# Kernel tuning notes

Hardware: AMD Instinct MI355X
Metric: run time of the kernel (lower is better)

## Reference

```python
import jax, jax.numpy as jnp
import numpy as np

N_EXP, N_EMBD = 8, 1024
D_FF = 4 * N_EMBD
TOK = 2048  # tokens per expert


def setup_inputs() -> dict:
    key = jax.random.key(0)
    k_x, k_fc, k_pr, k_fb, k_pb = jax.random.split(key, 5)
    scale = 0.02
    return {
        "x": jax.random.normal(k_x, (N_EXP, TOK, N_EMBD), dtype=jnp.float32),
        "c_fc": jax.random.normal(k_fc, (N_EXP, N_EMBD, D_FF), dtype=jnp.float32) * scale,
        "c_proj": jax.random.normal(k_pr, (N_EXP, D_FF, N_EMBD), dtype=jnp.float32) * scale,
        "fc_bias": jax.random.normal(k_fb, (N_EXP, 1, D_FF), dtype=jnp.float32) * scale,
        "proj_bias": jax.random.normal(k_pb, (N_EXP, 1, N_EMBD), dtype=jnp.float32) * scale,
    }


def reference(x, c_fc, c_proj, fc_bias, proj_bias):
    # grouped GEMM over experts: [e, t, d] @ [e, d, f] -> [e, t, f]
    h = jnp.einsum('etd,edf->etf', x, c_fc) + fc_bias
    h = jax.nn.gelu(h, approximate=False)  # torch nn.GELU default is exact erf
    out = jnp.einsum('etf,efd->etd', h, c_proj) + proj_bias
    # dropout p=0.0 (eval): identity
    return out
```

## Files before the change

### kernel.cpp

```cpp
#include <hip/hip_runtime.h>
#include <cmath>

typedef __bf16 bf16;
typedef __bf16 bf16x8 __attribute__((ext_vector_type(8)));
typedef float floatx4 __attribute__((ext_vector_type(4)));

#define E_ 8
#define M_ 2048
#define D_ 1024
#define F_ 4096

#define PUNROLL _Pragma("unroll")

__device__ __forceinline__ void async16(const void* g, void* l) {
    __builtin_amdgcn_global_load_lds((const __attribute__((address_space(1))) unsigned int*)g,
                                     (__attribute__((address_space(3))) unsigned int*)l, 16, 0, 0);
}

__device__ __forceinline__ float gelu_fast(float u) {
    float s = u * (-1.5957691216f - 0.0713548162726f * u * u);
    return u * __builtin_amdgcn_rcpf(1.0f + __expf(s));
}

__device__ __forceinline__ void tconv_body(const float* __restrict__ in, bf16* __restrict__ out,
                                           int R, int C, int bx, int by, int bz,
                                           float (*t)[65]) {
    size_t eoff = (size_t)bz * R * C;
    in += eoff;
    out += eoff;
    const int c0 = bx * 64, r0 = by * 64;
    const int tid = threadIdx.x;
    const int f4c = tid & 15;
    const int rsub = tid >> 4;
    PUNROLL
    for (int p = 0; p < 4; ++p) {
        int row = rsub + p * 16;
        float4 v = *(const float4*)&in[(size_t)(r0 + row) * C + c0 + f4c * 4];
        t[row][f4c * 4 + 0] = v.x;
        t[row][f4c * 4 + 1] = v.y;
        t[row][f4c * 4 + 2] = v.z;
        t[row][f4c * 4 + 3] = v.w;
    }
    __syncthreads();
    const int rr = (tid & 7) * 8;
    const int cbase = tid >> 3;
    PUNROLL
    for (int p = 0; p < 2; ++p) {
        int c = cbase + p * 32;
        bf16x8 o = {(bf16)t[rr + 0][c], (bf16)t[rr + 1][c], (bf16)t[rr + 2][c],
                    (bf16)t[rr + 3][c], (bf16)t[rr + 4][c], (bf16)t[rr + 5][c],
                    (bf16)t[rr + 6][c], (bf16)t[rr + 7][c]};
        *(bf16x8*)&out[(size_t)(c0 + c) * R + r0 + rr] = o;
    }
}

__global__ __launch_bounds__(256) void prep_kernel(const float4* __restrict__ x,
                                                   bf16x8* __restrict__ xb,
                                                   const float* __restrict__ c_fc,
                                                   bf16* __restrict__ w1T) {
    __shared__ float t[64][65];
    const int b = blockIdx.x;
    if (b < 2048) {
        const int n8 = E_ * M_ * D_ / 8;
        int i = b * 256 + threadIdx.x;
        for (; i < n8; i += 2048 * 256) {
            float4 a = x[2 * i], c = x[2 * i + 1];
            bf16x8 r = {(bf16)a.x, (bf16)a.y, (bf16)a.z, (bf16)a.w,
                        (bf16)c.x, (bf16)c.y, (bf16)c.z, (bf16)c.w};
            xb[i] = r;
        }
    } else {
        const int idx = b - 2048;
        tconv_body(c_fc, w1T, D_, F_, idx & 63, (idx >> 6) & 15, idx >> 10, t);
    }
}

__global__ __launch_bounds__(256) void tconv2_kernel(const float* __restrict__ in,
                                                     bf16* __restrict__ out) {
    __shared__ float t[64][65];
    const int idx = blockIdx.x;
    tconv_body(in, out, F_, D_, idx & 15, (idx >> 4) & 63, idx >> 10, t);
}

template <bool GELU>
__global__ __launch_bounds__(512, 2) void gemm256(const bf16* __restrict__ A,
                                                  const bf16* __restrict__ Bt,
                                                  const float* __restrict__ bias,
                                                  void* __restrict__ Out,
                                                  int M, int N, int K) {
    extern __shared__ __align__(16) char sm[];
    const int nt = K >> 6;
    const int NTm = M >> 8;
    const int NTn = N >> 8;
    const int nwg = gridDim.x;
    const int bid = blockIdx.x;
    const int swz = (bid & 7) * (nwg >> 3) + (bid >> 3);
    const int tm = swz % NTm;
    const int tn = (swz / NTm) % NTn;
    const int e = swz / (NTm * NTn);
    A += (size_t)e * M * K;
    Bt += (size_t)e * N * K;
    bias += (size_t)e * N;
    const int row0 = tm << 8;
    const int col0 = tn << 8;

    const int tid = threadIdx.x;
    const int l = tid & 63;
    const int w = tid >> 6;
    const int wm = w >> 2;
    const int wn = w & 3;

    const size_t Kb = (size_t)K * 2;
    const size_t half128 = 128 * Kb;
    const size_t j64 = 64 * Kb;
    const int srow = (w << 3) + (l >> 3);
    const int kb = ((l & 7) ^ ((l >> 3) & 7)) << 4;
    const char* aSrc = (const char*)A + (size_t)(row0 + srow) * Kb + kb;
    const char* bSrc = (const char*)Bt + (size_t)(col0 + srow) * Kb + kb;
    const int ldsW = w << 10;

    auto stage = [&](int hb, const char* src, int ko) {
        async16(src + ko, sm + hb + ldsW);
        async16(src + j64 + ko, sm + hb + 8192 + ldsW);
    };

    const int kpat0 = (((l >> 4) << 4)) ^ ((l & 7) << 4);
    const int kpat1 = (64 + ((l >> 4) << 4)) ^ ((l & 7) << 4);
    const int aRowOff = (((wm << 6) + (l & 15)) << 7);
    const int bRowOff = (((wn << 5) + (l & 15)) << 7);

    bf16x8 aa[4][2];
    bf16x8 bb0[2][2], bb1[2][2];
    floatx4 acc00[4][2] = {}, acc01[4][2] = {}, acc10[4][2] = {}, acc11[4][2] = {};

#define READ_A(QM)                                                                          \
    PUNROLL                                                                                 \
    for (int mi = 0; mi < 4; ++mi) {                                                        \
        aa[mi][0] = *(const bf16x8*)(sm + p + (QM)*16384 + aRowOff + mi * 2048 + kpat0);    \
        aa[mi][1] = *(const bf16x8*)(sm + p + (QM)*16384 + aRowOff + mi * 2048 + kpat1);    \
    }
#define READ_B(BB, QN)                                                                      \
    PUNROLL                                                                                 \
    for (int ni = 0; ni < 2; ++ni) {                                                        \
        BB[ni][0] = *(const bf16x8*)(sm + p + 32768 + (QN)*16384 + bRowOff + ni * 2048 + kpat0); \
        BB[ni][1] = *(const bf16x8*)(sm + p + 32768 + (QN)*16384 + bRowOff + ni * 2048 + kpat1); \
    }
#define MQ(ACC, BB)                                                                         \
    PUNROLL                                                                                 \
    for (int mi = 0; mi < 4; ++mi) PUNROLL for (int ni = 0; ni < 2; ++ni) {                 \
        ACC[mi][ni] = __builtin_amdgcn_mfma_f32_16x16x32_bf16(aa[mi][0], BB[ni][0], ACC[mi][ni], 0, 0, 0); \
        ACC[mi][ni] = __builtin_amdgcn_mfma_f32_16x16x32_bf16(aa[mi][1], BB[ni][1], ACC[mi][ni], 0, 0, 0); \
    }

    stage(0, aSrc, 0);
    stage(32768, bSrc, 0);
    stage(49152, bSrc + half128, 0);
    stage(16384, aSrc + half128, 0);
    stage(65536 + 0, aSrc, 128);
    stage(65536 + 32768, bSrc, 128);
    stage(65536 + 49152, bSrc + half128, 128);
    asm volatile("s_waitcnt vmcnt(6)" ::: "memory");
    __builtin_amdgcn_s_barrier();

    for (int t = 0; t < nt; ++t) {
        const int p = (t & 1) << 16;
        const int pn = p ^ 65536;
        const int ko1 = (t + 1) << 7;
        const int ko2 = (t + 2) << 7;
        READ_A(0)
        READ_B(bb0, 0)
        if (t + 1 < nt) stage(pn + 16384, aSrc + half128, ko1);
        __builtin_amdgcn_s_barrier();
        __builtin_amdgcn_s_setprio(1);
        MQ(acc00, bb0)
        __builtin_amdgcn_s_setprio(0);
        __builtin_amdgcn_s_barrier();
        READ_B(bb1, 1)
        if (t + 2 < nt) stage(p + 0, aSrc, ko2);
        __builtin_amdgcn_s_barrier();
        __builtin_amdgcn_s_setprio(1);
        MQ(acc01, bb1)
        __builtin_amdgcn_s_setprio(0);
        __builtin_amdgcn_s_barrier();
        READ_A(1)
        if (t + 2 < nt) stage(p + 32768, bSrc, ko2);
        __builtin_amdgcn_s_barrier();
        __builtin_amdgcn_s_setprio(1);
        MQ(acc11, bb1)
        __builtin_amdgcn_s_setprio(0);
        __builtin_amdgcn_s_barrier();
        if (t + 2 < nt) {
            stage(p + 49152, bSrc + half128, ko2);
            asm volatile("s_waitcnt vmcnt(6)" ::: "memory");
        } else if (t + 1 < nt) {
            asm volatile("s_waitcnt vmcnt(0)" ::: "memory");
        }
        __builtin_amdgcn_s_barrier();
        __builtin_amdgcn_s_setprio(1);
        MQ(acc10, bb0)
        __builtin_amdgcn_s_setprio(0);
        __builtin_amdgcn_s_barrier();
    }

    const size_t outBase = (size_t)e * M * N;
#define EPI(ACC, QM, QN)                                                                    \
    PUNROLL                                                                                 \
    for (int ni = 0; ni < 2; ++ni) {                                                        \
        const int col = col0 + (QN)*128 + (wn << 5) + ni * 16 + (l & 15);                   \
        const float bv = bias[col];                                                         \
        PUNROLL                                                                             \
        for (int mi = 0; mi < 4; ++mi) {                                                    \
            const int row = row0 + (QM)*128 + (wm << 6) + mi * 16 + ((l >> 4) << 2);        \
            PUNROLL                                                                         \
            for (int r = 0; r < 4; ++r) {                                                   \
                float v = ACC[mi][ni][r] + bv;                                              \
                if (GELU)                                                                   \
                    ((bf16*)Out)[outBase + (size_t)(row + r) * N + col] = (bf16)gelu_fast(v); \
                else                                                                        \
                    ((float*)Out)[outBase + (size_t)(row + r) * N + col] = v;               \
            }                                                                               \
        }                                                                                   \
    }
    EPI(acc00, 0, 0)
    EPI(acc01, 0, 1)
    EPI(acc11, 1, 1)
    EPI(acc10, 1, 0)
#undef READ_A
#undef READ_B
#undef MQ
#undef EPI
}

extern "C" void kernel_launch(void* const* d_in, const int* in_sizes, int n_in,
                              void* d_out, int out_size, void* d_ws, size_t ws_size,
                              hipStream_t stream) {
    const float* x = (const float*)d_in[0];
    const float* c_fc = (const float*)d_in[1];
    const float* c_proj = (const float*)d_in[2];
    const float* fc_bias = (const float*)d_in[3];
    const float* proj_bias = (const float*)d_in[4];
    float* out = (float*)d_out;

    bf16* xb = (bf16*)d_ws;
    bf16* wT = xb + (size_t)E_ * M_ * D_;
    bf16* h = wT + (size_t)E_ * D_ * F_;
    size_t need = ((size_t)E_ * M_ * D_ + (size_t)E_ * D_ * F_ + (size_t)E_ * M_ * F_) * 2;
    if (ws_size < need) return;

    static bool attrDone = false;
    if (!attrDone) {
        (void)hipFuncSetAttribute((const void*)&gemm256<true>,
                                  hipFuncAttributeMaxDynamicSharedMemorySize, 131072);
        (void)hipFuncSetAttribute((const void*)&gemm256<false>,
                                  hipFuncAttributeMaxDynamicSharedMemorySize, 131072);
        attrDone = true;
    }

    prep_kernel<<<10240, 256, 0, stream>>>((const float4*)x, (bf16x8*)xb, c_fc, wT);
    gemm256<true><<<1024, 512, 131072, stream>>>(xb, wT, fc_bias, h, M_, F_, D_);
    tconv2_kernel<<<8192, 256, 0, stream>>>(c_proj, wT);
    gemm256<false><<<256, 512, 131072, stream>>>(h, wT, proj_bias, out, M_, D_, F_);
}
```

Before: 613.3 us.

## Make GEMM persistent over tiles with overlapped next-tile prologue; fuse weight prep

The first GEMM now launches 256 workgroups that each loop over 4 output tiles. Each workgroup issues the async LDS prologue loads for its next tile before running the epilogue of the current one, so global loads overlap the output stores. When the workspace is large enough, both weight transposes and the x conversion are fused into one prep launch, which removes a kernel launch and the serialization between the GEMMs. The costs are tile-ordering and cache-locality changes from the new swizzle, plus extra workspace for a second transposed weight buffer.

```diff
diff --git a/kernel.cpp b/kernel.cpp
--- a/kernel.cpp
+++ b/kernel.cpp
@@ -54,6 +54,37 @@
     }
 }
 
+__device__ __forceinline__ void xconv_body(const float4* __restrict__ x, bf16x8* __restrict__ xb,
+                                           int b, int nblk) {
+    const int n8 = E_ * M_ * D_ / 8;
+    int i = b * 256 + threadIdx.x;
+    for (; i < n8; i += nblk * 256) {
+        float4 a = x[2 * i], c = x[2 * i + 1];
+        bf16x8 r = {(bf16)a.x, (bf16)a.y, (bf16)a.z, (bf16)a.w,
+                    (bf16)c.x, (bf16)c.y, (bf16)c.z, (bf16)c.w};
+        xb[i] = r;
+    }
+}
+
+__global__ __launch_bounds__(256) void prep_all(const float4* __restrict__ x,
+                                                bf16x8* __restrict__ xb,
+                                                const float* __restrict__ c_fc,
+                                                bf16* __restrict__ w1T,
+                                                const float* __restrict__ c_proj,
+                                                bf16* __restrict__ w2T) {
+    __shared__ float t[64][65];
+    const int b = blockIdx.x;
+    if (b < 2048) {
+        xconv_body(x, xb, b, 2048);
+    } else if (b < 10240) {
+        const int idx = b - 2048;
+        tconv_body(c_fc, w1T, D_, F_, idx & 63, (idx >> 6) & 15, idx >> 10, t);
+    } else {
+        const int idx = b - 10240;
+        tconv_body(c_proj, w2T, F_, D_, idx & 15, (idx >> 4) & 63, idx >> 10, t);
+    }
+}
+
 __global__ __launch_bounds__(256) void prep_kernel(const float4* __restrict__ x,
                                                    bf16x8* __restrict__ xb,
                                                    const float* __restrict__ c_fc,
@@ -61,14 +92,7 @@
     __shared__ float t[64][65];
     const int b = blockIdx.x;
     if (b < 2048) {
-        const int n8 = E_ * M_ * D_ / 8;
-        int i = b * 256 + threadIdx.x;
-        for (; i < n8; i += 2048 * 256) {
-            float4 a = x[2 * i], c = x[2 * i + 1];
-            bf16x8 r = {(bf16)a.x, (bf16)a.y, (bf16)a.z, (bf16)a.w,
-                        (bf16)c.x, (bf16)c.y, (bf16)c.z, (bf16)c.w};
-            xb[i] = r;
-        }
+        xconv_body(x, xb, b, 2048);
     } else {
         const int idx = b - 2048;
         tconv_body(c_fc, w1T, D_, F_, idx & 63, (idx >> 6) & 15, idx >> 10, t);
@@ -83,11 +107,11 @@
 }
 
 template <bool GELU>
-__global__ __launch_bounds__(512, 2) void gemm256(const bf16* __restrict__ A,
-                                                  const bf16* __restrict__ Bt,
-                                                  const float* __restrict__ bias,
+__global__ __launch_bounds__(512, 2) void gemm256(const bf16* __restrict__ A0,
+                                                  const bf16* __restrict__ Bt0,
+                                                  const float* __restrict__ bias0,
                                                   void* __restrict__ Out,
-                                                  int M, int N, int K) {
+                                                  int M, int N, int K, int tpb) {
     extern __shared__ __align__(16) char sm[];
     const int nt = K >> 6;
     const int NTm = M >> 8;
@@ -95,14 +119,6 @@
     const int nwg = gridDim.x;
     const int bid = blockIdx.x;
     const int swz = (bid & 7) * (nwg >> 3) + (bid >> 3);
-    const int tm = swz % NTm;
-    const int tn = (swz / NTm) % NTn;
-    const int e = swz / (NTm * NTn);
-    A += (size_t)e * M * K;
-    Bt += (size_t)e * N * K;
-    bias += (size_t)e * N;
-    const int row0 = tm << 8;
-    const int col0 = tn << 8;
 
     const int tid = threadIdx.x;
     const int l = tid & 63;
@@ -115,23 +131,42 @@
     const size_t j64 = 64 * Kb;
     const int srow = (w << 3) + (l >> 3);
     const int kb = ((l & 7) ^ ((l >> 3) & 7)) << 4;
-    const char* aSrc = (const char*)A + (size_t)(row0 + srow) * Kb + kb;
-    const char* bSrc = (const char*)Bt + (size_t)(col0 + srow) * Kb + kb;
     const int ldsW = w << 10;
 
     auto stage = [&](int hb, const char* src, int ko) {
         async16(src + ko, sm + hb + ldsW);
         async16(src + j64 + ko, sm + hb + 8192 + ldsW);
     };
+    auto prologue = [&](const char* aS, const char* bS) {
+        stage(0, aS, 0);
+        stage(32768, bS, 0);
+        stage(49152, bS + half128, 0);
+        stage(16384, aS + half128, 0);
+        stage(65536 + 0, aS, 128);
+        stage(65536 + 32768, bS, 128);
+        stage(65536 + 49152, bS + half128, 128);
+    };
 
     const int kpat0 = (((l >> 4) << 4)) ^ ((l & 7) << 4);
     const int kpat1 = (64 + ((l >> 4) << 4)) ^ ((l & 7) << 4);
     const int aRowOff = (((wm << 6) + (l & 15)) << 7);
     const int bRowOff = (((wn << 5) + (l & 15)) << 7);
 
-    bf16x8 aa[4][2];
-    bf16x8 bb0[2][2], bb1[2][2];
-    floatx4 acc00[4][2] = {}, acc01[4][2] = {}, acc10[4][2] = {}, acc11[4][2] = {};
+    int tile = swz * tpb;
+    int tm = tile % NTm, rem = tile / NTm;
+    int tn = rem % NTn, e = rem / NTn;
+    int row0 = tm << 8, col0 = tn << 8;
+    const char* aS = (const char*)A0 + ((size_t)e * M + row0 + srow) * Kb + kb;
+    const char* bS = (const char*)Bt0 + ((size_t)e * N + col0 + srow) * Kb + kb;
+    prologue(aS, bS);
+
+    for (int j = 0; j < tpb; ++j) {
+        asm volatile("s_waitcnt vmcnt(6)" ::: "memory");
+        __builtin_amdgcn_s_barrier();
+
+        bf16x8 aa[4][2];
+        bf16x8 bb0[2][2], bb1[2][2];
+        floatx4 acc00[4][2] = {}, acc01[4][2] = {}, acc10[4][2] = {}, acc11[4][2] = {};
 
 #define READ_A(QM)                                                                          \
     PUNROLL                                                                                 \
@@ -152,83 +187,86 @@
         ACC[mi][ni] = __builtin_amdgcn_mfma_f32_16x16x32_bf16(aa[mi][1], BB[ni][1], ACC[mi][ni], 0, 0, 0); \
     }
 
-    stage(0, aSrc, 0);
-    stage(32768, bSrc, 0);
-    stage(49152, bSrc + half128, 0);
-    stage(16384, aSrc + half128, 0);
-    stage(65536 + 0, aSrc, 128);
-    stage(65536 + 32768, bSrc, 128);
-    stage(65536 + 49152, bSrc + half128, 128);
-    asm volatile("s_waitcnt vmcnt(6)" ::: "memory");
-    __builtin_amdgcn_s_barrier();
-
-    for (int t = 0; t < nt; ++t) {
-        const int p = (t & 1) << 16;
-        const int pn = p ^ 65536;
-        const int ko1 = (t + 1) << 7;
-        const int ko2 = (t + 2) << 7;
-        READ_A(0)
-        READ_B(bb0, 0)
-        if (t + 1 < nt) stage(pn + 16384, aSrc + half128, ko1);
-        __builtin_amdgcn_s_barrier();
-        __builtin_amdgcn_s_setprio(1);
-        MQ(acc00, bb0)
-        __builtin_amdgcn_s_setprio(0);
-        __builtin_amdgcn_s_barrier();
-        READ_B(bb1, 1)
-        if (t + 2 < nt) stage(p + 0, aSrc, ko2);
-        __builtin_amdgcn_s_barrier();
-        __builtin_amdgcn_s_setprio(1);
-        MQ(acc01, bb1)
-        __builtin_amdgcn_s_setprio(0);
-        __builtin_amdgcn_s_barrier();
-        READ_A(1)
-        if (t + 2 < nt) stage(p + 32768, bSrc, ko2);
-        __builtin_amdgcn_s_barrier();
-        __builtin_amdgcn_s_setprio(1);
-        MQ(acc11, bb1)
-        __builtin_amdgcn_s_setprio(0);
-        __builtin_amdgcn_s_barrier();
-        if (t + 2 < nt) {
-            stage(p + 49152, bSrc + half128, ko2);
-            asm volatile("s_waitcnt vmcnt(6)" ::: "memory");
-        } else if (t + 1 < nt) {
-            asm volatile("s_waitcnt vmcnt(0)" ::: "memory");
+        for (int t = 0; t < nt; ++t) {
+            const int p = (t & 1) << 16;
+            const int pn = p ^ 65536;
+            const int ko1 = (t + 1) << 7;
+            const int ko2 = (t + 2) << 7;
+            READ_A(0)
+            READ_B(bb0, 0)
+            if (t + 1 < nt) stage(pn + 16384, aS + half128, ko1);
+            __builtin_amdgcn_s_barrier();
+            __builtin_amdgcn_s_setprio(1);
+            MQ(acc00, bb0)
+            __builtin_amdgcn_s_setprio(0);
+            __builtin_amdgcn_s_barrier();
+            READ_B(bb1, 1)
+            if (t + 2 < nt) stage(p + 0, aS, ko2);
+            __builtin_amdgcn_s_barrier();
+            __builtin_amdgcn_s_setprio(1);
+            MQ(acc01, bb1)
+            __builtin_amdgcn_s_setprio(0);
+            __builtin_amdgcn_s_barrier();
+            READ_A(1)
+            if (t + 2 < nt) stage(p + 32768, bS, ko2);
+            __builtin_amdgcn_s_barrier();
+            __builtin_amdgcn_s_setprio(1);
+            MQ(acc11, bb1)
+            __builtin_amdgcn_s_setprio(0);
+            __builtin_amdgcn_s_barrier();
+            if (t + 2 < nt) {
+                stage(p + 49152, bS + half128, ko2);
+                asm volatile("s_waitcnt vmcnt(6)" ::: "memory");
+            } else if (t + 1 < nt) {
+                asm volatile("s_waitcnt vmcnt(0)" ::: "memory");
+            }
+            __builtin_amdgcn_s_barrier();
+            __builtin_amdgcn_s_setprio(1);
+            MQ(acc10, bb0)
+            __builtin_amdgcn_s_setprio(0);
+            __builtin_amdgcn_s_barrier();
         }
-        __builtin_amdgcn_s_barrier();
-        __builtin_amdgcn_s_setprio(1);
-        MQ(acc10, bb0)
-        __builtin_amdgcn_s_setprio(0);
-        __builtin_amdgcn_s_barrier();
-    }
-
-    const size_t outBase = (size_t)e * M * N;
+
+        const int erow0 = row0, ecol0 = col0;
+        const float* ebias = bias0 + (size_t)e * N;
+        const size_t eout = (size_t)e * M * N;
+        if (j + 1 < tpb) {
+            tile = swz * tpb + j + 1;
+            tm = tile % NTm; rem = tile / NTm;
+            tn = rem % NTn; e = rem / NTn;
+            row0 = tm << 8; col0 = tn << 8;
+            aS = (const char*)A0 + ((size_t)e * M + row0 + srow) * Kb + kb;
+            bS = (const char*)Bt0 + ((size_t)e * N + col0 + srow) * Kb + kb;
+            prologue(aS, bS);
+        }
+
 #define EPI(ACC, QM, QN)                                                                    \
     PUNROLL                                                                                 \
     for (int ni = 0; ni < 2; ++ni) {                                                        \
-        const int col = col0 + (QN)*128 + (wn << 5) + ni * 16 + (l & 15);                   \
-        const float bv = bias[col];                                                         \
+        const int col = ecol0 + (QN)*128 + (wn << 5) + ni * 16 + (l & 15);                  \
+        const float bv = ebias[col];                                                        \
         PUNROLL                                                                             \
         for (int mi = 0; mi < 4; ++mi) {                                                    \
-            const int row = row0 + (QM)*128 + (wm << 6) + mi * 16 + ((l >> 4) << 2);        \
+            const int row = erow0 + (QM)*128 + (wm << 6) + mi * 16 + ((l >> 4) << 2);       \
             PUNROLL                                                                         \
             for (int r = 0; r < 4; ++r) {                                                   \
                 float v = ACC[mi][ni][r] + bv;                                              \
                 if (GELU)                                                                   \
-                    ((bf16*)Out)[outBase + (size_t)(row + r) * N + col] = (bf16)gelu_fast(v); \
+                    ((bf16*)Out)[eout + (size_t)(row + r) * N + col] = (bf16)gelu_fast(v);  \
                 else                                                                        \
-                    ((float*)Out)[outBase + (size_t)(row + r) * N + col] = v;               \
+                    ((float*)Out)[eout + (size_t)(row + r) * N + col] = v;                  \
             }                                                                               \
         }                                                                                   \
     }
-    EPI(acc00, 0, 0)
-    EPI(acc01, 0, 1)
-    EPI(acc11, 1, 1)
-    EPI(acc10, 1, 0)
+        EPI(acc00, 0, 0)
+        EPI(acc01, 0, 1)
+        EPI(acc11, 1, 1)
+        EPI(acc10, 1, 0)
 #undef READ_A
 #undef READ_B
 #undef MQ
 #undef EPI
+    }
 }
 
 extern "C" void kernel_launch(void* const* d_in, const int* in_sizes, int n_in,
@@ -241,11 +279,12 @@
     const float* proj_bias = (const float*)d_in[4];
     float* out = (float*)d_out;
 
-    bf16* xb = (bf16*)d_ws;
-    bf16* wT = xb + (size_t)E_ * M_ * D_;
-    bf16* h = wT + (size_t)E_ * D_ * F_;
-    size_t need = ((size_t)E_ * M_ * D_ + (size_t)E_ * D_ * F_ + (size_t)E_ * M_ * F_) * 2;
-    if (ws_size < need) return;
+    const size_t EMD = (size_t)E_ * M_ * D_;
+    const size_t EDF = (size_t)E_ * D_ * F_;
+    const size_t EMF = (size_t)E_ * M_ * F_;
+    const size_t need1 = (EMD + EDF + EMF) * 2;
+    const size_t need2 = (EMD + 2 * EDF + EMF) * 2;
+    if (ws_size < need1) return;
 
     static bool attrDone = false;
     if (!attrDone) {
@@ -256,8 +295,21 @@
         attrDone = true;
     }
 
-    prep_kernel<<<10240, 256, 0, stream>>>((const float4*)x, (bf16x8*)xb, c_fc, wT);
-    gemm256<true><<<1024, 512, 131072, stream>>>(xb, wT, fc_bias, h, M_, F_, D_);
-    tconv2_kernel<<<8192, 256, 0, stream>>>(c_proj, wT);
-    gemm256<false><<<256, 512, 131072, stream>>>(h, wT, proj_bias, out, M_, D_, F_);
-}
+    bf16* xb = (bf16*)d_ws;
+    bf16* w1T = xb + EMD;
+
+    if (ws_size >= need2) {
+        bf16* w2T = w1T + EDF;
+        bf16* h = w2T + EDF;
+        prep_all<<<18432, 256, 0, stream>>>((const float4*)x, (bf16x8*)xb, c_fc, w1T,
+                                            c_proj, w2T);
+        gemm256<true><<<256, 512, 131072, stream>>>(xb, w1T, fc_bias, h, M_, F_, D_, 4);
+        gemm256<false><<<256, 512, 131072, stream>>>(h, w2T, proj_bias, out, M_, D_, F_, 1);
+    } else {
+        bf16* h = w1T + EDF;
+        prep_kernel<<<10240, 256, 0, stream>>>((const float4*)x, (bf16x8*)xb, c_fc, w1T);
+        gemm256<true><<<256, 512, 131072, stream>>>(xb, w1T, fc_bias, h, M_, F_, D_, 4);
+        tconv2_kernel<<<8192, 256, 0, stream>>>(c_proj, w1T);
+        gemm256<false><<<256, 512, 131072, stream>>>(h, w1T, proj_bias, out, M_, D_, F_, 1);
+    }
+}
```

After: 608.2 us. No clear change (-0.8%).
